# Optimization experiments

Hardware: AMD Instinct MI355X
Metric: run time of the kernel (lower is better)

Reference implementation:

```python
import jax, jax.numpy as jnp
import numpy as np

N_NODES = 50000
N_HYPEREDGES = 50000
E = 320000
D = 256


def _prelu(x, a):
    return jnp.where(x >= 0, x, a * x)


def _hypergraph_conv(x, hei, W, b, num_nodes, num_edges):
    # PyG HypergraphConv, use_attention=False, heads=1:
    # out = D^{-1} H B^{-1} H^T (X W^T) + b
    src = hei[0]  # node indices, [E]
    he = hei[1]   # hyperedge indices, [E]
    xw = x @ W.T  # [N, D] node transform (lin has no bias)
    ones = jnp.ones((hei.shape[1],), x.dtype)
    deg_n = jax.ops.segment_sum(ones, src, num_segments=num_nodes)   # node degree D
    deg_e = jax.ops.segment_sum(ones, he, num_segments=num_edges)    # hyperedge size B
    d_inv = jnp.where(deg_n > 0, 1.0 / deg_n, 0.0)
    b_inv = jnp.where(deg_e > 0, 1.0 / deg_e, 0.0)
    # node -> hyperedge aggregation, scaled by B^{-1}
    edge_feat = b_inv[:, None] * jax.ops.segment_sum(xw[src], he, num_segments=num_edges)  # [n_he, D]
    # hyperedge -> node aggregation, scaled by D^{-1}
    out = d_inv[:, None] * jax.ops.segment_sum(edge_feat[he], src, num_segments=num_nodes)  # [N, D]
    return out + b


def setup_inputs() -> dict:
    key = jax.random.key(0)
    ks = jax.random.split(key, 6)
    std = np.sqrt(2.0 / D)  # kaiming_normal
    x = jax.random.normal(ks[0], (N_NODES, D), dtype=jnp.float32)
    hyper_edge_index = jax.random.randint(ks[1], (2, E), 0, N_HYPEREDGES, dtype=jnp.int64)
    W1 = jax.random.normal(ks[2], (D, D), dtype=jnp.float32) * std
    b1 = jnp.zeros((D,), jnp.float32)
    W2 = jax.random.normal(ks[3], (D, D), dtype=jnp.float32) * std
    b2 = jnp.zeros((D,), jnp.float32)
    prelu_a = jnp.asarray(0.25, jnp.float32)
    return {"x": x, "W1": W1, "b1": b1, "W2": W2, "b2": b2,
            "prelu_a": prelu_a, "hyper_edge_index": hyper_edge_index}


def reference(x, W1, b1, W2, b2, prelu_a, hyper_edge_index):
    out = _hypergraph_conv(x, hyper_edge_index, W1, b1, N_NODES, N_HYPEREDGES)
    out = _prelu(out, prelu_a)
    out = _hypergraph_conv(out, hyper_edge_index, W2, b2, N_NODES, N_HYPEREDGES)
    out = out + x  # residual
    out = _prelu(out, prelu_a)
    return out
```

## Files before the change

### kernel.cpp

```cpp
#include <hip/hip_runtime.h>

#define NN    50000
#define NHE   50000
#define NEDGE 320000
#define DD    256

#define SB    1024
#define NBLK  ((NN + SB - 1) / SB)

typedef float f32x4 __attribute__((ext_vector_type(4)));
typedef short short8 __attribute__((ext_vector_type(8)));

static __device__ __forceinline__ unsigned short f2b(float f) {
    union { float f; unsigned u; } c; c.f = f;
    unsigned u = c.u;
    u += 0x7fffu + ((u >> 16) & 1u);
    return (unsigned short)(u >> 16);
}
static __device__ __forceinline__ float b2f_lo(unsigned v) {
    union { unsigned u; float f; } c; c.u = v << 16; return c.f;
}
static __device__ __forceinline__ float b2f_hi(unsigned v) {
    union { unsigned u; float f; } c; c.u = v & 0xffff0000u; return c.f;
}
static __device__ __forceinline__ unsigned pack2(float a, float b) {
    return (unsigned)f2b(a) | ((unsigned)f2b(b) << 16);
}

__global__ __launch_bounds__(256) void k_count(const int* __restrict__ src,
                                               const int* __restrict__ he,
                                               int* __restrict__ cnt_n,
                                               int* __restrict__ cnt_e) {
    int e = blockIdx.x * 256 + threadIdx.x;
    if (e >= NEDGE) return;
    atomicAdd(&cnt_n[src[e]], 1);
    atomicAdd(&cnt_e[he[e]], 1);
}

__global__ __launch_bounds__(256) void k_scan_a(const int* __restrict__ cnt_n,
                                                const int* __restrict__ cnt_e,
                                                int* __restrict__ bsum) {
    int b   = blockIdx.x;
    int seg = b / NBLK, lb = b % NBLK;
    const int* cnt = seg ? cnt_e : cnt_n;
    int t = threadIdx.x;
    int idx = lb * SB + t * 4;
    int s = 0;
#pragma unroll
    for (int j = 0; j < 4; ++j)
        if (idx + j < NN) s += cnt[idx + j];
    __shared__ int red[256];
    red[t] = s;
    __syncthreads();
    for (int o = 128; o > 0; o >>= 1) {
        if (t < o) red[t] += red[t + o];
        __syncthreads();
    }
    if (t == 0) bsum[b] = red[0];
}

__global__ __launch_bounds__(64) void k_scan_b(const int* __restrict__ bsum,
                                               int* __restrict__ bbase) {
    if (threadIdx.x == 0) {
        int r = 0;
        for (int i = 0; i < NBLK; ++i) { bbase[i] = r; r += bsum[i]; }
        bbase[2 * NBLK] = r;
        r = 0;
        for (int i = NBLK; i < 2 * NBLK; ++i) { bbase[i] = r; r += bsum[i]; }
        bbase[2 * NBLK + 1] = r;
    }
}

__global__ __launch_bounds__(256) void k_scan_c(const int* __restrict__ cnt_n,
                                                const int* __restrict__ cnt_e,
                                                const int* __restrict__ bbase,
                                                int* __restrict__ off_n,
                                                int* __restrict__ off_e) {
    int b   = blockIdx.x;
    int seg = b / NBLK, lb = b % NBLK;
    const int* cnt = seg ? cnt_e : cnt_n;
    int* off = seg ? off_e : off_n;
    int t = threadIdx.x;
    int idx = lb * SB + t * 4;
    int v[4];
    int tsum = 0;
#pragma unroll
    for (int j = 0; j < 4; ++j) {
        v[j] = (idx + j < NN) ? cnt[idx + j] : 0;
        tsum += v[j];
    }
    __shared__ int sc[256];
    sc[t] = tsum;
    __syncthreads();
    for (int o = 1; o < 256; o <<= 1) {
        int val = (t >= o) ? sc[t - o] : 0;
        __syncthreads();
        sc[t] += val;
        __syncthreads();
    }
    int p = bbase[b] + sc[t] - tsum;
#pragma unroll
    for (int j = 0; j < 4; ++j) {
        if (idx + j < NN) off[idx + j] = p;
        p += v[j];
    }
    if (b == 0 && t == 0) off_n[NN] = bbase[2 * NBLK];
    if (b == NBLK && t == 0) off_e[NHE] = bbase[2 * NBLK + 1];
}

__global__ __launch_bounds__(256) void k_fill(const int* __restrict__ src,
                                              const int* __restrict__ he,
                                              const int* __restrict__ off_n,
                                              const int* __restrict__ off_e,
                                              int* __restrict__ cur_n,
                                              int* __restrict__ cur_e,
                                              int* __restrict__ adj_n,
                                              int* __restrict__ adj_e) {
    int e = blockIdx.x * 256 + threadIdx.x;
    if (e >= NEDGE) return;
    int s = src[e], h = he[e];
    int pn = off_n[s] + atomicAdd(&cur_n[s], 1);
    adj_n[pn] = h;
    int pe = off_e[h] + atomicAdd(&cur_e[h], 1);
    adj_e[pe] = s;
}

__global__ __launch_bounds__(256) void k_cvt_w(const float* __restrict__ w1,
                                               const float* __restrict__ w2,
                                               unsigned short* __restrict__ o1,
                                               unsigned short* __restrict__ o2) {
    int t = blockIdx.x * 256 + threadIdx.x;
    const int n4 = DD * DD / 4;
    const float* s = (t < n4) ? w1 : w2;
    unsigned short* d = (t < n4) ? o1 : o2;
    int i = (t < n4) ? t : t - n4;
    float4 v = ((const float4*)s)[i];
    uint2 o;
    o.x = pack2(v.x, v.y);
    o.y = pack2(v.z, v.w);
    ((uint2*)d)[i] = o;
}

template <bool A32>
__global__ __launch_bounds__(256) void k_gemm_bf16(const void* __restrict__ Av,
                                                   const unsigned short* __restrict__ Wb,
                                                   unsigned short* __restrict__ Cb, int M) {
    __shared__ __align__(16) unsigned short As[128 * 32];
    __shared__ __align__(16) unsigned short Bs[128 * 32];
    const int t    = threadIdx.x;
    const int m0   = blockIdx.x * 128;
    const int n0   = blockIdx.y * 128;
    const int lane = t & 63;
    const int wave = t >> 6;
    const int wm   = (wave >> 1) * 64;
    const int wn   = (wave & 1) * 64;
    const int fr   = lane & 15;
    const int fq   = lane >> 4;

    f32x4 acc[4][4] = {};

    const int sr = t >> 2;
    const int ss = t & 3;

    for (int k0 = 0; k0 < DD; k0 += 32) {
        __syncthreads();
#pragma unroll
        for (int i = 0; i < 2; ++i) {
            int r  = sr + i * 64;
            int gm = m0 + r;
            uint4 av = make_uint4(0u, 0u, 0u, 0u);
            if (gm < M) {
                if (A32) {
                    const float* p = (const float*)Av + (size_t)gm * DD + k0 + ss * 8;
                    float4 f0 = *(const float4*)p;
                    float4 f1 = *(const float4*)(p + 4);
                    av.x = pack2(f0.x, f0.y);
                    av.y = pack2(f0.z, f0.w);
                    av.z = pack2(f1.x, f1.y);
                    av.w = pack2(f1.z, f1.w);
                } else {
                    av = *(const uint4*)((const unsigned short*)Av + (size_t)gm * DD + k0 + ss * 8);
                }
            }
            *(uint4*)(As + r * 32 + ((ss ^ (r & 3)) * 8)) = av;
            uint4 bv = *(const uint4*)(Wb + (size_t)(n0 + r) * DD + k0 + ss * 8);
            *(uint4*)(Bs + r * 32 + ((ss ^ (r & 3)) * 8)) = bv;
        }
        __syncthreads();

        short8 af[4], bf[4];
#pragma unroll
        for (int mt = 0; mt < 4; ++mt) {
            int r = wm + mt * 16 + fr;
            af[mt] = *(const short8*)(As + r * 32 + ((fq ^ (r & 3)) * 8));
        }
#pragma unroll
        for (int nt = 0; nt < 4; ++nt) {
            int r = wn + nt * 16 + fr;
            bf[nt] = *(const short8*)(Bs + r * 32 + ((fq ^ (r & 3)) * 8));
        }
#pragma unroll
        for (int mt = 0; mt < 4; ++mt)
#pragma unroll
            for (int nt = 0; nt < 4; ++nt)
                acc[mt][nt] = __builtin_amdgcn_mfma_f32_16x16x32_bf16(af[mt], bf[nt],
                                                                      acc[mt][nt], 0, 0, 0);
    }

#pragma unroll
    for (int mt = 0; mt < 4; ++mt) {
#pragma unroll
        for (int i = 0; i < 4; ++i) {
            int gm = m0 + wm + mt * 16 + fq * 4 + i;
            if (gm >= M) continue;
#pragma unroll
            for (int nt = 0; nt < 4; ++nt) {
                int gn = n0 + wn + nt * 16 + fr;
                Cb[(size_t)gm * DD + gn] = f2b(acc[mt][nt][i]);
            }
        }
    }
}

static __device__ __forceinline__ void gather4(const unsigned short* __restrict__ srcb,
                                               const int* __restrict__ adj,
                                               int b, int e, int lane,
                                               float& a0, float& a1, float& a2, float& a3) {
    a0 = a1 = a2 = a3 = 0.f;
    for (int i = b; i < e; i += 4) {
        int g0 = adj[i];
        int g1 = (i + 1 < e) ? adj[i + 1] : g0;
        int g2 = (i + 2 < e) ? adj[i + 2] : g0;
        int g3 = (i + 3 < e) ? adj[i + 3] : g0;
        uint2 v0 = *(const uint2*)(srcb + (size_t)g0 * DD + lane * 4);
        uint2 v1 = *(const uint2*)(srcb + (size_t)g1 * DD + lane * 4);
        uint2 v2 = *(const uint2*)(srcb + (size_t)g2 * DD + lane * 4);
        uint2 v3 = *(const uint2*)(srcb + (size_t)g3 * DD + lane * 4);
        a0 += b2f_lo(v0.x); a1 += b2f_hi(v0.x); a2 += b2f_lo(v0.y); a3 += b2f_hi(v0.y);
        if (i + 1 < e) { a0 += b2f_lo(v1.x); a1 += b2f_hi(v1.x); a2 += b2f_lo(v1.y); a3 += b2f_hi(v1.y); }
        if (i + 2 < e) { a0 += b2f_lo(v2.x); a1 += b2f_hi(v2.x); a2 += b2f_lo(v2.y); a3 += b2f_hi(v2.y); }
        if (i + 3 < e) { a0 += b2f_lo(v3.x); a1 += b2f_hi(v3.x); a2 += b2f_lo(v3.y); a3 += b2f_hi(v3.y); }
    }
}

__global__ __launch_bounds__(256) void k_gather_edge_b(const unsigned short* __restrict__ xw,
                                                       unsigned short* __restrict__ ef,
                                                       const int* __restrict__ off,
                                                       const int* __restrict__ adj) {
    int w = (blockIdx.x * 256 + threadIdx.x) >> 6;
    int lane = threadIdx.x & 63;
    if (w >= NHE) return;
    int b = off[w], e = off[w + 1];
    float a0, a1, a2, a3;
    gather4(xw, adj, b, e, lane, a0, a1, a2, a3);
    float sc = (e > b) ? 1.f / (float)(e - b) : 0.f;
    uint2 o;
    o.x = pack2(a0 * sc, a1 * sc);
    o.y = pack2(a2 * sc, a3 * sc);
    *(uint2*)(ef + (size_t)w * DD + lane * 4) = o;
}

__global__ __launch_bounds__(256) void k_gather_node_mid_b(const unsigned short* __restrict__ ef,
                                                           unsigned short* __restrict__ h,
                                                           const int* __restrict__ off,
                                                           const int* __restrict__ adj,
                                                           const float* __restrict__ bias,
                                                           const float* __restrict__ aP) {
    int w = (blockIdx.x * 256 + threadIdx.x) >> 6;
    int lane = threadIdx.x & 63;
    if (w >= NN) return;
    int b = off[w], e = off[w + 1];
    float a0, a1, a2, a3;
    gather4(ef, adj, b, e, lane, a0, a1, a2, a3);
    float sc = (e > b) ? 1.f / (float)(e - b) : 0.f;
    float a = *aP;
    float4 bb = ((const float4*)bias)[lane];
    float r0 = a0 * sc + bb.x; r0 = (r0 >= 0.f) ? r0 : a * r0;
    float r1 = a1 * sc + bb.y; r1 = (r1 >= 0.f) ? r1 : a * r1;
    float r2 = a2 * sc + bb.z; r2 = (r2 >= 0.f) ? r2 : a * r2;
    float r3 = a3 * sc + bb.w; r3 = (r3 >= 0.f) ? r3 : a * r3;
    uint2 o;
    o.x = pack2(r0, r1);
    o.y = pack2(r2, r3);
    *(uint2*)(h + (size_t)w * DD + lane * 4) = o;
}

__global__ __launch_bounds__(256) void k_gather_node_final_b(const unsigned short* __restrict__ ef,
                                                             const float* __restrict__ x,
                                                             float* __restrict__ out,
                                                             const int* __restrict__ off,
                                                             const int* __restrict__ adj,
                                                             const float* __restrict__ bias,
                                                             const float* __restrict__ aP) {
    int w = (blockIdx.x * 256 + threadIdx.x) >> 6;
    int lane = threadIdx.x & 63;
    if (w >= NN) return;
    int b = off[w], e = off[w + 1];
    float a0, a1, a2, a3;
    gather4(ef, adj, b, e, lane, a0, a1, a2, a3);
    float sc = (e > b) ? 1.f / (float)(e - b) : 0.f;
    float a = *aP;
    float4 bb = ((const float4*)bias)[lane];
    float4 xv = *(const float4*)(x + (size_t)w * DD + lane * 4);
    float4 r;
    r.x = a0 * sc + bb.x + xv.x; r.x = (r.x >= 0.f) ? r.x : a * r.x;
    r.y = a1 * sc + bb.y + xv.y; r.y = (r.y >= 0.f) ? r.y : a * r.y;
    r.z = a2 * sc + bb.z + xv.z; r.z = (r.z >= 0.f) ? r.z : a * r.z;
    r.w = a3 * sc + bb.w + xv.w; r.w = (r.w >= 0.f) ? r.w : a * r.w;
    *(float4*)(out + (size_t)w * DD + lane * 4) = r;
}

extern "C" void kernel_launch(void* const* d_in, const int* in_sizes, int n_in,
                              void* d_out, int out_size, void* d_ws, size_t ws_size,
                              hipStream_t stream) {
    const float* x       = (const float*)d_in[0];
    const float* W1      = (const float*)d_in[1];
    const float* b1      = (const float*)d_in[2];
    const float* W2      = (const float*)d_in[3];
    const float* b2      = (const float*)d_in[4];
    const float* prelu_a = (const float*)d_in[5];
    const int*   hei     = (const int*)d_in[6];
    const int* idx_src = hei;
    const int* idx_he  = hei + NEDGE;

    float* out = (float*)d_out;
    unsigned short* B1 = (unsigned short*)d_ws;
    unsigned short* B2 = B1 + (size_t)NN * DD;
    int* off_n = (int*)(B2 + (size_t)NN * DD);
    int* off_e = off_n + NN + 1;
    int* cur_n = off_e + NHE + 1;
    int* cur_e = cur_n + NN;
    int* adj_n = cur_e + NHE;
    int* adj_e = adj_n + NEDGE;
    int* bsum  = adj_e + NEDGE;
    int* bbase = bsum + 2 * NBLK;
    unsigned short* w1b = (unsigned short*)d_out;
    unsigned short* w2b = w1b + DD * DD;

    const int eblocks = (NEDGE + 255) / 256;
    const int gblocks = (NN * 64 + 255) / 256;
    dim3 ggrid((NN + 127) / 128, DD / 128);

    hipMemsetAsync(cur_n, 0, sizeof(int) * (NN + NHE), stream);
    k_count<<<eblocks, 256, 0, stream>>>(idx_src, idx_he, cur_n, cur_e);
    k_scan_a<<<2 * NBLK, 256, 0, stream>>>(cur_n, cur_e, bsum);
    k_scan_b<<<1, 64, 0, stream>>>(bsum, bbase);
    k_scan_c<<<2 * NBLK, 256, 0, stream>>>(cur_n, cur_e, bbase, off_n, off_e);
    hipMemsetAsync(cur_n, 0, sizeof(int) * (NN + NHE), stream);
    k_fill<<<eblocks, 256, 0, stream>>>(idx_src, idx_he, off_n, off_e,
                                        cur_n, cur_e, adj_n, adj_e);

    k_cvt_w<<<(2 * DD * DD / 4 + 255) / 256, 256, 0, stream>>>(W1, W2, w1b, w2b);

    k_gemm_bf16<true><<<ggrid, 256, 0, stream>>>((const void*)x, w1b, B1, NN);
    k_gather_edge_b<<<gblocks, 256, 0, stream>>>(B1, B2, off_e, adj_e);
    k_gather_node_mid_b<<<gblocks, 256, 0, stream>>>(B2, B1, off_n, adj_n, b1, prelu_a);

    k_gemm_bf16<false><<<ggrid, 256, 0, stream>>>((const void*)B1, w2b, B2, NN);
    k_gather_edge_b<<<gblocks, 256, 0, stream>>>(B2, B1, off_e, adj_e);
    k_gather_node_final_b<<<gblocks, 256, 0, stream>>>(B1, x, out, off_n, adj_n, b2, prelu_a);
}
```

Baseline: 364.7 us.

## Double-buffer GEMM LDS tiles and widen gather loads to 16 bytes per lane

The bf16 GEMM now uses two LDS buffers and prefetches the next K-slice into registers while the MFMAs on the current slice run, leaving one barrier per iteration. The three gather kernels now use 32 lanes per row, each loading 8 bf16 values with a 16-byte load, so two rows share a wave. This halves the number of launched threads and gives each load more bytes and each thread more independent work. The cost is more registers and LDS in the GEMM, and fewer lanes per row in the gathers.

```diff
diff --git a/kernel.cpp b/kernel.cpp
--- a/kernel.cpp
+++ b/kernel.cpp
@@ -145,8 +145,8 @@
 __global__ __launch_bounds__(256) void k_gemm_bf16(const void* __restrict__ Av,
                                                    const unsigned short* __restrict__ Wb,
                                                    unsigned short* __restrict__ Cb, int M) {
-    __shared__ __align__(16) unsigned short As[128 * 32];
-    __shared__ __align__(16) unsigned short Bs[128 * 32];
+    __shared__ __align__(16) unsigned short As[2][128 * 32];
+    __shared__ __align__(16) unsigned short Bs[2][128 * 32];
     const int t    = threadIdx.x;
     const int m0   = blockIdx.x * 128;
     const int n0   = blockIdx.y * 128;
@@ -162,8 +162,8 @@
     const int sr = t >> 2;
     const int ss = t & 3;
 
-    for (int k0 = 0; k0 < DD; k0 += 32) {
-        __syncthreads();
+    uint4 pa[2], pb[2];
+    auto loadT = [&](int k0, uint4* ra, uint4* rb) {
 #pragma unroll
         for (int i = 0; i < 2; ++i) {
             int r  = sr + i * 64;
@@ -182,22 +182,39 @@
                     av = *(const uint4*)((const unsigned short*)Av + (size_t)gm * DD + k0 + ss * 8);
                 }
             }
-            *(uint4*)(As + r * 32 + ((ss ^ (r & 3)) * 8)) = av;
-            uint4 bv = *(const uint4*)(Wb + (size_t)(n0 + r) * DD + k0 + ss * 8);
-            *(uint4*)(Bs + r * 32 + ((ss ^ (r & 3)) * 8)) = bv;
+            ra[i] = av;
+            rb[i] = *(const uint4*)(Wb + (size_t)(n0 + r) * DD + k0 + ss * 8);
         }
+    };
+    auto storeT = [&](int buf, const uint4* ra, const uint4* rb) {
+#pragma unroll
+        for (int i = 0; i < 2; ++i) {
+            int r = sr + i * 64;
+            *(uint4*)(As[buf] + r * 32 + ((ss ^ (r & 3)) * 8)) = ra[i];
+            *(uint4*)(Bs[buf] + r * 32 + ((ss ^ (r & 3)) * 8)) = rb[i];
+        }
+    };
+
+    loadT(0, pa, pb);
+    storeT(0, pa, pb);
+
+#pragma unroll
+    for (int kk = 0; kk < 8; ++kk) {
         __syncthreads();
-
+        uint4 na[2], nb[2];
+        if (kk < 7) loadT((kk + 1) * 32, na, nb);
+
+        const int buf = kk & 1;
         short8 af[4], bf[4];
 #pragma unroll
         for (int mt = 0; mt < 4; ++mt) {
             int r = wm + mt * 16 + fr;
-            af[mt] = *(const short8*)(As + r * 32 + ((fq ^ (r & 3)) * 8));
+            af[mt] = *(const short8*)(As[buf] + r * 32 + ((fq ^ (r & 3)) * 8));
         }
 #pragma unroll
         for (int nt = 0; nt < 4; ++nt) {
             int r = wn + nt * 16 + fr;
-            bf[nt] = *(const short8*)(Bs + r * 32 + ((fq ^ (r & 3)) * 8));
+            bf[nt] = *(const short8*)(Bs[buf] + r * 32 + ((fq ^ (r & 3)) * 8));
         }
 #pragma unroll
         for (int mt = 0; mt < 4; ++mt)
@@ -205,6 +222,7 @@
             for (int nt = 0; nt < 4; ++nt)
                 acc[mt][nt] = __builtin_amdgcn_mfma_f32_16x16x32_bf16(af[mt], bf[nt],
                                                                       acc[mt][nt], 0, 0, 0);
+        if (kk < 7) storeT(1 - buf, na, nb);
     }
 
 #pragma unroll
@@ -222,24 +240,30 @@
     }
 }
 
-static __device__ __forceinline__ void gather4(const unsigned short* __restrict__ srcb,
+static __device__ __forceinline__ void acc8(float* a, uint4 v) {
+    a[0] += b2f_lo(v.x); a[1] += b2f_hi(v.x);
+    a[2] += b2f_lo(v.y); a[3] += b2f_hi(v.y);
+    a[4] += b2f_lo(v.z); a[5] += b2f_hi(v.z);
+    a[6] += b2f_lo(v.w); a[7] += b2f_hi(v.w);
+}
+static __device__ __forceinline__ void gather8(const unsigned short* __restrict__ srcb,
                                                const int* __restrict__ adj,
-                                               int b, int e, int lane,
-                                               float& a0, float& a1, float& a2, float& a3) {
-    a0 = a1 = a2 = a3 = 0.f;
+                                               int b, int e, int sl, float* a) {
+#pragma unroll
+    for (int i = 0; i < 8; ++i) a[i] = 0.f;
     for (int i = b; i < e; i += 4) {
         int g0 = adj[i];
         int g1 = (i + 1 < e) ? adj[i + 1] : g0;
         int g2 = (i + 2 < e) ? adj[i + 2] : g0;
         int g3 = (i + 3 < e) ? adj[i + 3] : g0;
-        uint2 v0 = *(const uint2*)(srcb + (size_t)g0 * DD + lane * 4);
-        uint2 v1 = *(const uint2*)(srcb + (size_t)g1 * DD + lane * 4);
-        uint2 v2 = *(const uint2*)(srcb + (size_t)g2 * DD + lane * 4);
-        uint2 v3 = *(const uint2*)(srcb + (size_t)g3 * DD + lane * 4);
-        a0 += b2f_lo(v0.x); a1 += b2f_hi(v0.x); a2 += b2f_lo(v0.y); a3 += b2f_hi(v0.y);
-        if (i + 1 < e) { a0 += b2f_lo(v1.x); a1 += b2f_hi(v1.x); a2 += b2f_lo(v1.y); a3 += b2f_hi(v1.y); }
-        if (i + 2 < e) { a0 += b2f_lo(v2.x); a1 += b2f_hi(v2.x); a2 += b2f_lo(v2.y); a3 += b2f_hi(v2.y); }
-        if (i + 3 < e) { a0 += b2f_lo(v3.x); a1 += b2f_hi(v3.x); a2 += b2f_lo(v3.y); a3 += b2f_hi(v3.y); }
+        uint4 v0 = *(const uint4*)(srcb + (size_t)g0 * DD + sl * 8);
+        uint4 v1 = *(const uint4*)(srcb + (size_t)g1 * DD + sl * 8);
+        uint4 v2 = *(const uint4*)(srcb + (size_t)g2 * DD + sl * 8);
+        uint4 v3 = *(const uint4*)(srcb + (size_t)g3 * DD + sl * 8);
+        acc8(a, v0);
+        if (i + 1 < e) acc8(a, v1);
+        if (i + 2 < e) acc8(a, v2);
+        if (i + 3 < e) acc8(a, v3);
     }
 }
 
@@ -247,17 +271,20 @@
                                                        unsigned short* __restrict__ ef,
                                                        const int* __restrict__ off,
                                                        const int* __restrict__ adj) {
-    int w = (blockIdx.x * 256 + threadIdx.x) >> 6;
-    int lane = threadIdx.x & 63;
+    int tid = blockIdx.x * 256 + threadIdx.x;
+    int w = tid >> 5;
+    int sl = tid & 31;
     if (w >= NHE) return;
     int b = off[w], e = off[w + 1];
-    float a0, a1, a2, a3;
-    gather4(xw, adj, b, e, lane, a0, a1, a2, a3);
+    float a[8];
+    gather8(xw, adj, b, e, sl, a);
     float sc = (e > b) ? 1.f / (float)(e - b) : 0.f;
-    uint2 o;
-    o.x = pack2(a0 * sc, a1 * sc);
-    o.y = pack2(a2 * sc, a3 * sc);
-    *(uint2*)(ef + (size_t)w * DD + lane * 4) = o;
+    uint4 o;
+    o.x = pack2(a[0] * sc, a[1] * sc);
+    o.y = pack2(a[2] * sc, a[3] * sc);
+    o.z = pack2(a[4] * sc, a[5] * sc);
+    o.w = pack2(a[6] * sc, a[7] * sc);
+    *(uint4*)(ef + (size_t)w * DD + sl * 8) = o;
 }
 
 __global__ __launch_bounds__(256) void k_gather_node_mid_b(const unsigned short* __restrict__ ef,
@@ -266,23 +293,30 @@
                                                            const int* __restrict__ adj,
                                                            const float* __restrict__ bias,
                                                            const float* __restrict__ aP) {
-    int w = (blockIdx.x * 256 + threadIdx.x) >> 6;
-    int lane = threadIdx.x & 63;
+    int tid = blockIdx.x * 256 + threadIdx.x;
+    int w = tid >> 5;
+    int sl = tid & 31;
     if (w >= NN) return;
     int b = off[w], e = off[w + 1];
-    float a0, a1, a2, a3;
-    gather4(ef, adj, b, e, lane, a0, a1, a2, a3);
+    float a[8];
+    gather8(ef, adj, b, e, sl, a);
     float sc = (e > b) ? 1.f / (float)(e - b) : 0.f;
-    float a = *aP;
-    float4 bb = ((const float4*)bias)[lane];
-    float r0 = a0 * sc + bb.x; r0 = (r0 >= 0.f) ? r0 : a * r0;
-    float r1 = a1 * sc + bb.y; r1 = (r1 >= 0.f) ? r1 : a * r1;
-    float r2 = a2 * sc + bb.z; r2 = (r2 >= 0.f) ? r2 : a * r2;
-    float r3 = a3 * sc + bb.w; r3 = (r3 >= 0.f) ? r3 : a * r3;
-    uint2 o;
-    o.x = pack2(r0, r1);
-    o.y = pack2(r2, r3);
-    *(uint2*)(h + (size_t)w * DD + lane * 4) = o;
+    float al = *aP;
+    float4 bb0 = ((const float4*)bias)[sl * 2];
+    float4 bb1 = ((const float4*)bias)[sl * 2 + 1];
+    float r[8];
+    r[0] = a[0] * sc + bb0.x; r[1] = a[1] * sc + bb0.y;
+    r[2] = a[2] * sc + bb0.z; r[3] = a[3] * sc + bb0.w;
+    r[4] = a[4] * sc + bb1.x; r[5] = a[5] * sc + bb1.y;
+    r[6] = a[6] * sc + bb1.z; r[7] = a[7] * sc + bb1.w;
+#pragma unroll
+    for (int i = 0; i < 8; ++i) r[i] = (r[i] >= 0.f) ? r[i] : al * r[i];
+    uint4 o;
+    o.x = pack2(r[0], r[1]);
+    o.y = pack2(r[2], r[3]);
+    o.z = pack2(r[4], r[5]);
+    o.w = pack2(r[6], r[7]);
+    *(uint4*)(h + (size_t)w * DD + sl * 8) = o;
 }
 
 __global__ __launch_bounds__(256) void k_gather_node_final_b(const unsigned short* __restrict__ ef,
@@ -292,22 +326,30 @@
                                                              const int* __restrict__ adj,
                                                              const float* __restrict__ bias,
                                                              const float* __restrict__ aP) {
-    int w = (blockIdx.x * 256 + threadIdx.x) >> 6;
-    int lane = threadIdx.x & 63;
+    int tid = blockIdx.x * 256 + threadIdx.x;
+    int w = tid >> 5;
+    int sl = tid & 31;
     if (w >= NN) return;
     int b = off[w], e = off[w + 1];
-    float a0, a1, a2, a3;
-    gather4(ef, adj, b, e, lane, a0, a1, a2, a3);
+    float a[8];
+    gather8(ef, adj, b, e, sl, a);
     float sc = (e > b) ? 1.f / (float)(e - b) : 0.f;
-    float a = *aP;
-    float4 bb = ((const float4*)bias)[lane];
-    float4 xv = *(const float4*)(x + (size_t)w * DD + lane * 4);
-    float4 r;
-    r.x = a0 * sc + bb.x + xv.x; r.x = (r.x >= 0.f) ? r.x : a * r.x;
-    r.y = a1 * sc + bb.y + xv.y; r.y = (r.y >= 0.f) ? r.y : a * r.y;
-    r.z = a2 * sc + bb.z + xv.z; r.z = (r.z >= 0.f) ? r.z : a * r.z;
-    r.w = a3 * sc + bb.w + xv.w; r.w = (r.w >= 0.f) ? r.w : a * r.w;
-    *(float4*)(out + (size_t)w * DD + lane * 4) = r;
+    float al = *aP;
+    float4 bb0 = ((const float4*)bias)[sl * 2];
+    float4 bb1 = ((const float4*)bias)[sl * 2 + 1];
+    const float* xp = x + (size_t)w * DD + sl * 8;
+    float4 xv0 = *(const float4*)xp;
+    float4 xv1 = *(const float4*)(xp + 4);
+    float r[8];
+    r[0] = a[0] * sc + bb0.x + xv0.x; r[1] = a[1] * sc + bb0.y + xv0.y;
+    r[2] = a[2] * sc + bb0.z + xv0.z; r[3] = a[3] * sc + bb0.w + xv0.w;
+    r[4] = a[4] * sc + bb1.x + xv1.x; r[5] = a[5] * sc + bb1.y + xv1.y;
+    r[6] = a[6] * sc + bb1.z + xv1.z; r[7] = a[7] * sc + bb1.w + xv1.w;
+#pragma unroll
+    for (int i = 0; i < 8; ++i) r[i] = (r[i] >= 0.f) ? r[i] : al * r[i];
+    float* op = out + (size_t)w * DD + sl * 8;
+    *(float4*)op = make_float4(r[0], r[1], r[2], r[3]);
+    *(float4*)(op + 4) = make_float4(r[4], r[5], r[6], r[7]);
 }
 
 extern "C" void kernel_launch(void* const* d_in, const int* in_sizes, int n_in,
@@ -338,7 +380,7 @@
     unsigned short* w2b = w1b + DD * DD;
 
     const int eblocks = (NEDGE + 255) / 256;
-    const int gblocks = (NN * 64 + 255) / 256;
+    const int gblocks = (NN * 32 + 255) / 256;
     dim3 ggrid((NN + 127) / 128, DD / 128);
 
     hipMemsetAsync(cur_n, 0, sizeof(int) * (NN + NHE), stream);
```

New measurement: 370.9 us. Within noise of the previous version (+1.7%).
